# Optimization experiments

Hardware: AMD Instinct MI355X
Metric: run time of the kernel (lower is better)

Reference implementation:

```python
import jax, jax.numpy as jnp
import numpy as np

BATCH, SEQ, DIM, NUM_CODES = 8, 2048, 1024, 8192

def setup_inputs() -> dict:
    key = jax.random.key(0)
    kx, kc = jax.random.split(key)
    x = jax.random.normal(kx, (BATCH, SEQ, DIM), dtype=jnp.float32)
    # nn.Embedding default init: N(0, 1)
    codebook = jax.random.normal(kc, (NUM_CODES, DIM), dtype=jnp.float32)
    return {"x": x, "codebook": codebook}

def reference(x, codebook):
    # tau=0 path of CodebookLayer.forward (SnapFunction.forward):
    # similarity logits [B, S, num_codes], nearest-code argmax, gather.
    logits = jnp.einsum('bsd,cd->bsc', x, codebook)
    codebook_ids = jnp.argmax(logits, axis=-1)            # [B, S] int
    output = jnp.take(codebook, codebook_ids, axis=0)     # [B, S, D]
    return output
```

## Files before the change

### kernel.cpp

```cpp
#include <hip/hip_runtime.h>
#include <stdint.h>


#define T_TOKENS 16384
#define N_CODES  8192
#define DIM      1024
#define BM 256
#define BN 256
#define BK 64
#define NBLK (N_CODES / BM)
#define KITERS (DIM / BK)
#define EPS 13.0f
#define MAXCAND 48

typedef int   int8v  __attribute__((ext_vector_type(8)));
typedef int   int4v  __attribute__((ext_vector_type(4)));
typedef float f32x16 __attribute__((ext_vector_type(16)));

#define GLD16(gp, lp) \
  __builtin_amdgcn_global_load_lds((__attribute__((address_space(1))) void*)(gp), \
                                   (__attribute__((address_space(3))) void*)(lp), 16, 0, 0)

__device__ inline uint32_t umax(uint32_t a, uint32_t b) { return a > b ? a : b; }
__device__ inline uint32_t umin(uint32_t a, uint32_t b) { return a < b ? a : b; }
__device__ inline uint32_t umed3(uint32_t a, uint32_t b, uint32_t c) {
  return umax(umin(a, b), umin(umax(a, b), c));
}

__device__ inline uint32_t f32_key(float v) {
  int32_t b = (int32_t)__float_as_uint(v);
  return (uint32_t)(b ^ ((b >> 31) | (int32_t)0x80000000));
}
__device__ inline float key_f32(uint32_t u) {
  uint32_t b = (u & 0x80000000u) ? (u & 0x7FFFFFFFu) : ~u;
  return __uint_as_float(b);
}

__global__ __launch_bounds__(256) void vq_prep(const float* __restrict__ x,
                                               const float* __restrict__ cbm,
                                               uint8_t* __restrict__ xq,
                                               uint8_t* __restrict__ cq) {
  size_t b = blockIdx.x;
  const float* src; uint8_t* dst;
  if (b < 16384) { src = x;  dst = xq; }
  else           { b -= 16384; src = cbm; dst = cq; }
  const size_t i = b * 256 + threadIdx.x;
  const float4 v = ((const float4*)src)[i];
  uint32_t r = __builtin_amdgcn_cvt_pk_fp8_f32(v.x, v.y, 0, false);
  r = __builtin_amdgcn_cvt_pk_fp8_f32(v.z, v.w, (int)r, true);
  ((uint32_t*)dst)[i] = r;
}

#define MFMA8(A_, B_, C_) \
  __builtin_amdgcn_mfma_scale_f32_32x32x64_f8f6f4((A_), (B_), (C_), 0, 0, 0, \
                                                  0x7F7F7F7F, 0, 0x7F7F7F7F)

__global__ __launch_bounds__(512) void vq_gemm_top3(
    const uint8_t* __restrict__ cq,
    const uint8_t* __restrict__ xq,
    uint32_t* __restrict__ pk)
{
  __shared__ uint8_t smem[4 * 32768];

  const int t    = threadIdx.x;
  const int wave = t >> 6;
  const int lane = t & 63;
  const int col  = lane & 31;
  const int hi   = lane >> 5;
  const int wm   = wave >> 2;
  const int wn2  = (wave & 3) * 64;

  const int f   = blockIdx.x;
  const int swz = (f & 7) * 256 + (f >> 3);
  const int cyi = swz >> 6;
  const int tb0 = (swz & 63) * BN;
  const int cb0 = cyi * BM;

  const int r0 = t >> 2;
  const int js = ((t & 3) ^ ((r0 >> 1) & 3)) * 16;
  const uint8_t* sA0 = cq + (size_t)(cb0 + r0) * DIM + js;
  const uint8_t* sA1 = cq + (size_t)(cb0 + r0 + 128) * DIM + js;
  const uint8_t* sB0 = xq + (size_t)(tb0 + r0) * DIM + js;
  const uint8_t* sB1 = xq + (size_t)(tb0 + r0 + 128) * DIM + js;

#define STAGE(bi, ti) do {                                     \
    uint8_t* Ad_ = smem + ((bi) << 15);                        \
    const int ko_ = (ti) * BK;                                 \
    GLD16(sA0 + ko_, Ad_ + t * 16);                            \
    GLD16(sA1 + ko_, Ad_ + (t + 512) * 16);                    \
    GLD16(sB0 + ko_, Ad_ + 16384 + t * 16);                    \
    GLD16(sB1 + ko_, Ad_ + 16384 + (t + 512) * 16);            \
  } while (0)

  const int j0 = hi * 2;
  int aoff[4][2], boff[2][2];
#pragma unroll
  for (int mi = 0; mi < 4; ++mi) {
    const int ra = wm * 128 + mi * 32 + col;
    const int pa = (ra >> 1) & 3;
    aoff[mi][0] = ra * 64 + (j0 ^ pa) * 16;
    aoff[mi][1] = ra * 64 + ((j0 + 1) ^ pa) * 16;
  }
#pragma unroll
  for (int jj = 0; jj < 2; ++jj) {
    const int rb = wn2 + jj * 32 + col;
    const int pb = (rb >> 1) & 3;
    boff[jj][0] = 16384 + rb * 64 + (j0 ^ pb) * 16;
    boff[jj][1] = 16384 + rb * 64 + ((j0 + 1) ^ pb) * 16;
  }

#define READ8(dst_, o0_, o1_) do {                                         \
    const int4v lo_ = *(const int4v*)(cur + (o0_));                        \
    const int4v hq_ = *(const int4v*)(cur + (o1_));                        \
    dst_ = (int8v){lo_[0], lo_[1], lo_[2], lo_[3],                         \
                   hq_[0], hq_[1], hq_[2], hq_[3]};                        \
  } while (0)

  f32x16 acc[4][2];
#pragma unroll
  for (int i = 0; i < 4; ++i)
#pragma unroll
    for (int j = 0; j < 2; ++j)
#pragma unroll
      for (int r = 0; r < 16; ++r) acc[i][j][r] = 0.f;

  STAGE(0, 0);
  STAGE(1, 1);

#pragma unroll 4
  for (int kt = 0; kt < KITERS; ++kt) {
    asm volatile("s_waitcnt vmcnt(4)" ::: "memory");
    __builtin_amdgcn_s_barrier();
    __builtin_amdgcn_sched_barrier(0);

    const uint8_t* cur = smem + ((kt & 3) << 15);
    STAGE((kt + 2) & 3, (kt + 2) & 15);

    int8v a[4], b0, b1;
#pragma unroll
    for (int mi = 0; mi < 4; ++mi) READ8(a[mi], aoff[mi][0], aoff[mi][1]);
    READ8(b0, boff[0][0], boff[0][1]);
    __builtin_amdgcn_s_barrier();
    asm volatile("s_waitcnt lgkmcnt(0)" ::: "memory");
    __builtin_amdgcn_sched_barrier(0);
    __builtin_amdgcn_s_setprio(1);
    acc[0][0] = MFMA8(a[0], b0, acc[0][0]);
    acc[1][0] = MFMA8(a[1], b0, acc[1][0]);
    acc[2][0] = MFMA8(a[2], b0, acc[2][0]);
    acc[3][0] = MFMA8(a[3], b0, acc[3][0]);
    __builtin_amdgcn_s_setprio(0);
    __builtin_amdgcn_s_barrier();

    READ8(b1, boff[1][0], boff[1][1]);
    __builtin_amdgcn_s_barrier();
    asm volatile("s_waitcnt lgkmcnt(0)" ::: "memory");
    __builtin_amdgcn_sched_barrier(0);
    __builtin_amdgcn_s_setprio(1);
    acc[0][1] = MFMA8(a[0], b1, acc[0][1]);
    acc[1][1] = MFMA8(a[1], b1, acc[1][1]);
    acc[2][1] = MFMA8(a[2], b1, acc[2][1]);
    acc[3][1] = MFMA8(a[3], b1, acc[3][1]);
    __builtin_amdgcn_s_setprio(0);
  }
  __syncthreads();

  uint32_t* cand = (uint32_t*)(smem + 2 * 32768);
  const int invb = 255 - wm * 128 - 4 * hi;
#pragma unroll
  for (int j = 0; j < 2; ++j) {
    uint32_t K1 = 0, K2 = 0, K3 = 0;
#pragma unroll
    for (int mi = 0; mi < 4; ++mi) {
#pragma unroll
      for (int rg = 0; rg < 16; ++rg) {
        const int rowoff = (rg & 3) + 8 * (rg >> 2);
        const uint32_t key = (f32_key(acc[mi][j][rg]) & 0xFFFFFF00u)
                           | (uint32_t)(invb - mi * 32 - rowoff);
        const uint32_t t3 = umed3(key, K2, K3);
        const uint32_t t2 = umed3(key, K1, K2);
        K1 = umax(key, K1); K2 = t2; K3 = t3;
      }
    }
    const uint32_t o1 = __shfl_xor(K1, 32, 64);
    const uint32_t o2 = __shfl_xor(K2, 32, 64);
    const uint32_t o3 = __shfl_xor(K3, 32, 64);
    const uint32_t m1 = umin(K1, o1), M2 = umax(K2, o2);
    const uint32_t m2 = umin(K2, o2), M3 = umax(K3, o3);
    K1 = umax(K1, o1);
    const uint32_t nk2 = umax(m1, M2);
    K3 = umax(umax(m2, umin(m1, M2)), M3);
    K2 = nk2;
    if (hi == 0) {
      uint32_t* c = &cand[((wn2 + j * 32 + col) * 2 + wm) * 3];
      c[0] = K1; c[1] = K2; c[2] = K3;
    }
  }
  __syncthreads();
  if (t < BN) {
    const uint32_t a1 = cand[(t * 2 + 0) * 3 + 0], a2 = cand[(t * 2 + 0) * 3 + 1],
                   a3 = cand[(t * 2 + 0) * 3 + 2];
    const uint32_t b1k = cand[(t * 2 + 1) * 3 + 0], b2 = cand[(t * 2 + 1) * 3 + 1],
                   b3 = cand[(t * 2 + 1) * 3 + 2];
    const uint32_t m1 = umin(a1, b1k), M2 = umax(a2, b2);
    const uint32_t m2 = umin(a2, b2), M3 = umax(a3, b3);
    uint32_t* dst = pk + ((size_t)(tb0 + t) * NBLK + cyi) * 3;
    dst[0] = umax(a1, b1k);
    dst[1] = umax(m1, M2);
    dst[2] = umax(umax(m2, umin(m1, M2)), M3);
  }
#undef STAGE
#undef READ8
}

__global__ __launch_bounds__(256) void vq_reduce_gather(
    const uint32_t* __restrict__ pk, const float* __restrict__ x,
    const float* __restrict__ cb, float* __restrict__ out)
{
  __shared__ float xs[DIM];
  __shared__ uint32_t wmax[4];
  __shared__ int scand[MAXCAND];
  __shared__ int scnt;
  __shared__ double sdot[MAXCAND];
  __shared__ int sbesti;

  const int tkn = blockIdx.x, t = threadIdx.x, lane = t & 63, wv = t >> 6;
  ((float4*)xs)[t] = ((const float4*)(x + (size_t)tkn * DIM))[t];
  const uint32_t key = (t < 3 * NBLK) ? pk[(size_t)tkn * (3 * NBLK) + t] : 0u;
  uint32_t m = key;
#pragma unroll
  for (int d = 1; d < 64; d <<= 1) m = umax(m, __shfl_xor(m, d, 64));
  if (t == 0) scnt = 0;
  if (lane == 0) wmax[wv] = m;
  __syncthreads();
  const float Mv = key_f32(umax(umax(wmax[0], wmax[1]), umax(wmax[2], wmax[3])));
  if (t < 3 * NBLK && key_f32(key) >= Mv - EPS) {
    const int p = atomicAdd(&scnt, 1);
    if (p < MAXCAND) scand[p] = (t / 3) * BM + 255 - (int)(key & 255u);
  }
  __syncthreads();
  const int cnt = scnt < MAXCAND ? scnt : MAXCAND;

  if (cnt > 1) {
    for (int k = wv; k < cnt; k += 4) {
      const int c = scand[k];
      const float* cr = cb + (size_t)c * DIM;
      double s = 0.0;
#pragma unroll
      for (int q = 0; q < 4; ++q) {
        const float4 xv = ((const float4*)xs)[lane + 64 * q];
        const float4 cv = ((const float4*)cr)[lane + 64 * q];
        s += (double)xv.x * cv.x + (double)xv.y * cv.y
           + (double)xv.z * cv.z + (double)xv.w * cv.w;
      }
#pragma unroll
      for (int d = 1; d < 64; d <<= 1) s += __shfl_xor(s, d, 64);
      if (lane == 0) sdot[k] = s;
    }
    __syncthreads();
    if (t == 0) {
      double best = -1e300; int bi = N_CODES;
      for (int k = 0; k < cnt; ++k) {
        const int c = scand[k];
        if (sdot[k] > best || (sdot[k] == best && c < bi)) { best = sdot[k]; bi = c; }
      }
      sbesti = bi;
    }
  } else {
    if (t == 0) sbesti = scand[0];
  }
  __syncthreads();
  const int code = sbesti;
  ((float4*)(out + (size_t)tkn * DIM))[t] = ((const float4*)(cb + (size_t)code * DIM))[t];
}

__global__ __launch_bounds__(256) void vq_naive(const float* __restrict__ x,
                                                const float* __restrict__ cb,
                                                float* __restrict__ out) {
  __shared__ float xs[DIM];
  __shared__ float bv[256];
  __shared__ int   bix[256];
  const int tkn = blockIdx.x;
  const int t = threadIdx.x;
  for (int d = t; d < DIM; d += 256) xs[d] = x[(size_t)tkn * DIM + d];
  __syncthreads();
  float best = -1e30f; int bi = N_CODES;
  for (int c = t; c < N_CODES; c += 256) {
    const float* cr = cb + (size_t)c * DIM;
    float s = 0.f;
    for (int d = 0; d < DIM; ++d) s += xs[d] * cr[d];
    if (s > best || (s == best && c < bi)) { best = s; bi = c; }
  }
  bv[t] = best; bix[t] = bi;
  __syncthreads();
  for (int off = 128; off > 0; off >>= 1) {
    if (t < off) {
      if (bv[t + off] > bv[t] || (bv[t + off] == bv[t] && bix[t + off] < bix[t])) {
        bv[t] = bv[t + off]; bix[t] = bix[t + off];
      }
    }
    __syncthreads();
  }
  const int code = bix[0];
  for (int d = t; d < DIM; d += 256)
    out[(size_t)tkn * DIM + d] = cb[(size_t)code * DIM + d];
}

extern "C" void kernel_launch(void* const* d_in, const int* in_sizes, int n_in,
                              void* d_out, int out_size, void* d_ws, size_t ws_size,
                              hipStream_t stream) {
  const float* x  = (const float*)d_in[0];
  const float* cb = (const float*)d_in[1];
  float* out = (float*)d_out;

  const size_t MB = 1024 * 1024;
  const size_t need = 24 * MB + (size_t)T_TOKENS * NBLK * 3 * 4;
  if (ws_size >= need) {
    uint8_t*  xq = (uint8_t*)d_ws;
    uint8_t*  cq = xq + 16 * MB;
    uint32_t* pk = (uint32_t*)(cq + 8 * MB);

    vq_prep<<<dim3(24576), 256, 0, stream>>>(x, cb, xq, cq);
    vq_gemm_top3<<<dim3((T_TOKENS / BN) * (N_CODES / BM)), 512, 0, stream>>>(cq, xq, pk);
    vq_reduce_gather<<<dim3(T_TOKENS), 256, 0, stream>>>(pk, x, cb, out);
  } else {
    vq_naive<<<dim3(T_TOKENS), 256, 0, stream>>>(x, cb, out);
  }
}
```

Measured before the change: 352.9 us.

## Load token operand directly into registers from global, staging only codebook in LDS

New measurement: 395.6 us. 1.12x slower.

```diff
diff --git a/kernel.cpp b/kernel.cpp
--- a/kernel.cpp
+++ b/kernel.cpp
@@ -60,7 +60,7 @@
     const uint8_t* __restrict__ xq,
     uint32_t* __restrict__ pk)
 {
-  __shared__ uint8_t smem[4 * 32768];
+  __shared__ uint8_t smem[4 * 16384];
 
   const int t    = threadIdx.x;
   const int wave = t >> 6;
@@ -80,20 +80,18 @@
   const int js = ((t & 3) ^ ((r0 >> 1) & 3)) * 16;
   const uint8_t* sA0 = cq + (size_t)(cb0 + r0) * DIM + js;
   const uint8_t* sA1 = cq + (size_t)(cb0 + r0 + 128) * DIM + js;
-  const uint8_t* sB0 = xq + (size_t)(tb0 + r0) * DIM + js;
-  const uint8_t* sB1 = xq + (size_t)(tb0 + r0 + 128) * DIM + js;
 
 #define STAGE(bi, ti) do {                                     \
-    uint8_t* Ad_ = smem + ((bi) << 15);                        \
-    const int ko_ = (ti) * BK;                                 \
-    GLD16(sA0 + ko_, Ad_ + t * 16);                            \
-    GLD16(sA1 + ko_, Ad_ + (t + 512) * 16);                    \
-    GLD16(sB0 + ko_, Ad_ + 16384 + t * 16);                    \
-    GLD16(sB1 + ko_, Ad_ + 16384 + (t + 512) * 16);            \
+    uint8_t* Ad_ = smem + ((bi) << 14);                        \
+    GLD16(sA0 + (ti) * BK, Ad_ + t * 16);                      \
+    GLD16(sA1 + (ti) * BK, Ad_ + (t + 512) * 16);              \
   } while (0)
 
+  const uint8_t* pB0 = xq + (size_t)(tb0 + wn2 + col) * DIM + hi * 32;
+  const uint8_t* pB1 = pB0 + (size_t)32 * DIM;
+
   const int j0 = hi * 2;
-  int aoff[4][2], boff[2][2];
+  int aoff[4][2];
 #pragma unroll
   for (int mi = 0; mi < 4; ++mi) {
     const int ra = wm * 128 + mi * 32 + col;
@@ -101,19 +99,11 @@
     aoff[mi][0] = ra * 64 + (j0 ^ pa) * 16;
     aoff[mi][1] = ra * 64 + ((j0 + 1) ^ pa) * 16;
   }
-#pragma unroll
-  for (int jj = 0; jj < 2; ++jj) {
-    const int rb = wn2 + jj * 32 + col;
-    const int pb = (rb >> 1) & 3;
-    boff[jj][0] = 16384 + rb * 64 + (j0 ^ pb) * 16;
-    boff[jj][1] = 16384 + rb * 64 + ((j0 + 1) ^ pb) * 16;
-  }
 
 #define READ8(dst_, o0_, o1_) do {                                         \
     const int4v lo_ = *(const int4v*)(cur + (o0_));                        \
     const int4v hq_ = *(const int4v*)(cur + (o1_));                        \
-    dst_ = (int8v){lo_[0], lo_[1], lo_[2], lo_[3],                         \
-                   hq_[0], hq_[1], hq_[2], hq_[3]};                        \
+    dst_ = __builtin_shufflevector(lo_, hq_, 0, 1, 2, 3, 4, 5, 6, 7);      \
   } while (0)
 
   f32x16 acc[4][2];
@@ -127,44 +117,43 @@
   STAGE(0, 0);
   STAGE(1, 1);
 
-#pragma unroll 4
+#pragma unroll
   for (int kt = 0; kt < KITERS; ++kt) {
-    asm volatile("s_waitcnt vmcnt(4)" ::: "memory");
+    asm volatile("s_waitcnt vmcnt(2)" ::: "memory");
     __builtin_amdgcn_s_barrier();
-    __builtin_amdgcn_sched_barrier(0);
-
-    const uint8_t* cur = smem + ((kt & 3) << 15);
-    STAGE((kt + 2) & 3, (kt + 2) & 15);
-
-    int8v a[4], b0, b1;
+    asm volatile("" ::: "memory");
+
+    const uint8_t* cur = smem + ((kt & 3) << 14);
+
+    int8v b0, b1;
+    {
+      const int4v l0 = *(const int4v*)(pB0 + kt * BK);
+      const int4v h0 = *(const int4v*)(pB0 + kt * BK + 16);
+      const int4v l1 = *(const int4v*)(pB1 + kt * BK);
+      const int4v h1 = *(const int4v*)(pB1 + kt * BK + 16);
+      b0 = __builtin_shufflevector(l0, h0, 0, 1, 2, 3, 4, 5, 6, 7);
+      b1 = __builtin_shufflevector(l1, h1, 0, 1, 2, 3, 4, 5, 6, 7);
+    }
+    asm volatile("" ::: "memory");
+
+    if (kt < KITERS - 2) STAGE((kt + 2) & 3, kt + 2);
+
+    int8v a[4];
 #pragma unroll
     for (int mi = 0; mi < 4; ++mi) READ8(a[mi], aoff[mi][0], aoff[mi][1]);
-    READ8(b0, boff[0][0], boff[0][1]);
-    __builtin_amdgcn_s_barrier();
-    asm volatile("s_waitcnt lgkmcnt(0)" ::: "memory");
-    __builtin_amdgcn_sched_barrier(0);
-    __builtin_amdgcn_s_setprio(1);
+
     acc[0][0] = MFMA8(a[0], b0, acc[0][0]);
     acc[1][0] = MFMA8(a[1], b0, acc[1][0]);
+    acc[0][1] = MFMA8(a[0], b1, acc[0][1]);
+    acc[1][1] = MFMA8(a[1], b1, acc[1][1]);
     acc[2][0] = MFMA8(a[2], b0, acc[2][0]);
     acc[3][0] = MFMA8(a[3], b0, acc[3][0]);
-    __builtin_amdgcn_s_setprio(0);
-    __builtin_amdgcn_s_barrier();
-
-    READ8(b1, boff[1][0], boff[1][1]);
-    __builtin_amdgcn_s_barrier();
-    asm volatile("s_waitcnt lgkmcnt(0)" ::: "memory");
-    __builtin_amdgcn_sched_barrier(0);
-    __builtin_amdgcn_s_setprio(1);
-    acc[0][1] = MFMA8(a[0], b1, acc[0][1]);
-    acc[1][1] = MFMA8(a[1], b1, acc[1][1]);
     acc[2][1] = MFMA8(a[2], b1, acc[2][1]);
     acc[3][1] = MFMA8(a[3], b1, acc[3][1]);
-    __builtin_amdgcn_s_setprio(0);
-  }
-  __syncthreads();
-
-  uint32_t* cand = (uint32_t*)(smem + 2 * 32768);
+  }
+  __syncthreads();
+
+  uint32_t* cand = (uint32_t*)smem;
   const int invb = 255 - wm * 128 - 4 * hi;
 #pragma unroll
   for (int j = 0; j < 2; ++j) {
```
